# Kernel tuning notes

Hardware: AMD Instinct MI355X
Metric: run time of the kernel (lower is better)

## Reference

```python
import jax, jax.numpy as jnp
import numpy as np

D_MODEL = 1024
D_K = 64
D_V = 64
N_HEADS = 16
LN_EPS = 1e-5


def setup_inputs() -> dict:
    key = jax.random.key(0)
    ks = jax.random.split(key, 9)
    B, S = 2, 2048
    scale = 0.02
    return {
        "input_Q": jax.random.normal(ks[0], (B, S, D_MODEL), dtype=jnp.float32),
        "input_K": jax.random.normal(ks[1], (B, S, D_MODEL), dtype=jnp.float32),
        "input_V": jax.random.normal(ks[2], (B, S, D_MODEL), dtype=jnp.float32),
        "W_Q": jax.random.normal(ks[3], (D_MODEL, N_HEADS * D_K), dtype=jnp.float32) * scale,
        "W_K": jax.random.normal(ks[4], (D_MODEL, N_HEADS * D_K), dtype=jnp.float32) * scale,
        "W_V": jax.random.normal(ks[5], (D_MODEL, N_HEADS * D_V), dtype=jnp.float32) * scale,
        "W_O": jax.random.normal(ks[6], (N_HEADS * D_V, D_MODEL), dtype=jnp.float32) * scale,
        "ln_gamma": jnp.ones((D_MODEL,), dtype=jnp.float32),
        "ln_beta": jnp.zeros((D_MODEL,), dtype=jnp.float32),
    }


def reference(input_Q, input_K, input_V, W_Q, W_K, W_V, W_O, ln_gamma, ln_beta):
    B, Lq, _ = input_Q.shape
    Lk = input_K.shape[1]
    # projections -> [B, H, L, d]
    Q = (input_Q @ W_Q).reshape(B, Lq, N_HEADS, D_K).transpose(0, 2, 1, 3)
    K = (input_K @ W_K).reshape(B, Lk, N_HEADS, D_K).transpose(0, 2, 1, 3)
    V = (input_V @ W_V).reshape(B, Lk, N_HEADS, D_V).transpose(0, 2, 1, 3)
    # scores: [B, H, Lq, Lk]
    scores = jnp.einsum("bhqd,bhkd->bhqk", Q, K) / jnp.sqrt(jnp.float32(D_K))
    # NOTE: source uses nn.Softmax(dim=1) -> softmax over the HEADS axis (faithful quirk)
    attn = jax.nn.softmax(scores, axis=1)
    context = jnp.einsum("bhqk,bhkv->bhqv", attn, V)
    context = context.transpose(0, 2, 1, 3).reshape(B, Lq, N_HEADS * D_V)
    output = context @ W_O
    # residual + LayerNorm over last dim
    x = output + input_Q
    mu = jnp.mean(x, axis=-1, keepdims=True)
    var = jnp.mean(jnp.square(x - mu), axis=-1, keepdims=True)
    return (x - mu) / jnp.sqrt(var + LN_EPS) * ln_gamma + ln_beta
```

## Files before the change

### kernel.cpp

```cpp
#include <hip/hip_runtime.h>
#include <cstdint>
#include <cstddef>

#define DM 1024
#define HEADS 16
#define DHEAD 64
#define SEQ 2048
#define BATCH 2

typedef __bf16 bf16x8 __attribute__((ext_vector_type(8)));
typedef float  f32x4  __attribute__((ext_vector_type(4)));
typedef unsigned short u16;
typedef unsigned int u32;
typedef u16 u16x8 __attribute__((ext_vector_type(8)));
typedef u16 u16x4 __attribute__((ext_vector_type(4)));

__device__ __forceinline__ float bf2f(u16 u){
    union { u32 i; float f; } v; v.i = ((u32)u) << 16; return v.f;
}
__device__ __forceinline__ u16 f2bf(float f){
    union { float f; u32 i; } v; v.f = f;
    u32 r = v.i + 0x7FFF + ((v.i >> 16) & 1);
    return (u16)(r >> 16);
}
__device__ __forceinline__ u16 f2bf_rhu(float f){
    union { float f; u32 i; } v; v.f = f;
    return (u16)((v.i + 0x8000u) >> 16);
}
__device__ __forceinline__ float fexp2(float x){
    float r;
    asm volatile("v_exp_f32 %0, %1\n\ts_nop 1" : "=v"(r) : "v"(x));
    return r;
}
__device__ __forceinline__ void gload16(const u16* g, u16* l){
    __builtin_amdgcn_global_load_lds(
        (const __attribute__((address_space(1))) u32*)g,
        (__attribute__((address_space(3))) u32*)l, 16, 0, 0);
}

__global__ void k_probe(const u16* __restrict__ q, int* __restrict__ hdr){
    if (threadIdx.x == 0 && blockIdx.x == 0){
        int cnt = 0;
        for (int i = 0; i < 256; i += 2){
            int e = (q[i] >> 7) & 0xFF;
            if (e >= 90 && e <= 141) cnt++;
        }
        hdr[0] = (cnt >= 64) ? 1 : 0;
        #pragma unroll
        for (int c = 1; c <= 24; c++) hdr[c] = 0;
    }
}

__global__ __launch_bounds__(256) void k_cvt3(const void* __restrict__ s0,
                                              const void* __restrict__ s1,
                                              const void* __restrict__ s2,
                                              u16* __restrict__ dstbase,
                                              const int* __restrict__ flag, int n){
    int z = blockIdx.y;
    const void* src = (z == 0) ? s0 : ((z == 1) ? s1 : s2);
    u16* dst = dstbase + (size_t)z * n;
    int i = (blockIdx.x * 256 + threadIdx.x) * 8;
    if (i >= n) return;
    if (*flag){
        *(u16x8*)&dst[i] = *(const u16x8*)((const u16*)src + i);
    } else {
        const float* s = (const float*)src + i;
        u16x8 o;
        #pragma unroll
        for (int j = 0; j < 8; j++) o[j] = f2bf(s[j]);
        *(u16x8*)&dst[i] = o;
    }
}

__global__ void k_tcvt4(const void* __restrict__ w0, const void* __restrict__ w1,
                        const void* __restrict__ w2, const void* __restrict__ w3,
                        u16* __restrict__ dstbase,
                        const int* __restrict__ flag, int R, int C){
    __shared__ u16 tile[32][33];
    int z = blockIdx.z;
    const void* src = (z == 0) ? w0 : ((z == 1) ? w1 : ((z == 2) ? w2 : w3));
    u16* dst = dstbase + (size_t)z * R * C;
    bool isbf = (*flag != 0);
    int c0 = blockIdx.x * 32, r0 = blockIdx.y * 32;
    int tx = threadIdx.x, ty = threadIdx.y;
    #pragma unroll
    for (int i = 0; i < 32; i += 8){
        size_t idx = (size_t)(r0 + ty + i) * C + c0 + tx;
        tile[ty + i][tx] = isbf ? ((const u16*)src)[idx] : f2bf(((const float*)src)[idx]);
    }
    __syncthreads();
    #pragma unroll
    for (int i = 0; i < 32; i += 8)
        dst[(size_t)(c0 + ty + i) * R + r0 + tx] = tile[tx][ty + i];
}

__global__ void k_transpose(const u16* __restrict__ src, u16* __restrict__ dst,
                            int R, int C){
    __shared__ u16 tile[32][33];
    size_t boff = (size_t)blockIdx.z * R * C;
    src += boff; dst += boff;
    int c0 = blockIdx.x * 32, r0 = blockIdx.y * 32;
    int tx = threadIdx.x, ty = threadIdx.y;
    #pragma unroll
    for (int i = 0; i < 32; i += 8)
        tile[ty + i][tx] = src[(size_t)(r0 + ty + i) * C + c0 + tx];
    __syncthreads();
    #pragma unroll
    for (int i = 0; i < 32; i += 8)
        dst[(size_t)(c0 + ty + i) * R + r0 + tx] = tile[tx][ty + i];
}

template<int NJ>
__global__ __launch_bounds__(256, 2) void k_gemmT(const u16* __restrict__ A0,
                                                  const u16* __restrict__ Bt0,
                                                  u16* __restrict__ C0,
                                                  size_t strA, size_t strB, size_t strC,
                                                  int M, int N, int K){
    constexpr int BN = NJ * 32;
    __shared__ u16 lsA[128 * 64];
    __shared__ u16 lsB[BN * 64];
    int z = blockIdx.z;
    const u16* A  = A0  + strA * z;
    const u16* Bt = Bt0 + strB * z;
    u16* C = C0 + strC * z;
    int m0 = blockIdx.y * 128, n0 = blockIdx.x * BN;
    int t = threadIdx.x, lane = t & 63, w = t >> 6;
    int l15 = lane & 15, quad = lane >> 4;
    int wm = (w & 1) * 64, wn = (w >> 1) * (NJ * 16);
    f32x4 acc[4][NJ] = {};
    for (int k0 = 0; k0 < K; k0 += 64){
        __syncthreads();
        #pragma unroll
        for (int j = 0; j < 4; j++){
            int ub = j * 256 + w * 64;
            int u  = ub + lane;
            int r  = u >> 3, cg = (u & 7) ^ (r & 7);
            gload16(&A[(size_t)(m0 + r) * K + k0 + cg * 8], &lsA[ub * 8]);
        }
        #pragma unroll
        for (int j = 0; j < NJ; j++){
            int ub = j * 256 + w * 64;
            int u  = ub + lane;
            int r  = u >> 3, cg = (u & 7) ^ (r & 7);
            gload16(&Bt[(size_t)(n0 + r) * K + k0 + cg * 8], &lsB[ub * 8]);
        }
        __syncthreads();
        bf16x8 af[4][2], bfr[NJ][2];
        #pragma unroll
        for (int i = 0; i < 4; i++){
            int row = wm + i * 16 + l15;
            #pragma unroll
            for (int kk = 0; kk < 2; kk++)
                af[i][kk] = *(const bf16x8*)&lsA[row * 64 + (((kk * 4 + quad) ^ (row & 7)) * 8)];
        }
        #pragma unroll
        for (int jj = 0; jj < NJ; jj++){
            int row = wn + jj * 16 + l15;
            #pragma unroll
            for (int kk = 0; kk < 2; kk++)
                bfr[jj][kk] = *(const bf16x8*)&lsB[row * 64 + (((kk * 4 + quad) ^ (row & 7)) * 8)];
        }
        #pragma unroll
        for (int i = 0; i < 4; i++)
            #pragma unroll
            for (int jj = 0; jj < NJ; jj++)
                #pragma unroll
                for (int kk = 0; kk < 2; kk++)
                    acc[i][jj] = __builtin_amdgcn_mfma_f32_16x16x32_bf16(af[i][kk], bfr[jj][kk],
                                                                         acc[i][jj], 0, 0, 0);
    }
    #pragma unroll
    for (int i = 0; i < 4; i++)
        #pragma unroll
        for (int jj = 0; jj < NJ; jj++)
            #pragma unroll
            for (int r = 0; r < 4; r++){
                int m = m0 + wm + i * 16 + quad * 4 + r;
                int n = n0 + wn + jj * 16 + l15;
                C[(size_t)m * N + n] = f2bf(acc[i][jj][r]);
            }
}

__global__ __launch_bounds__(1024, 4) void k_attn5(const u16* __restrict__ Qp,
                                                   const u16* __restrict__ Kp,
                                                   const u16* __restrict__ Vt,
                                                   u16* __restrict__ c0,
                                                   u16* __restrict__ c1,
                                                   u16* __restrict__ c2,
                                                   u16* __restrict__ c3,
                                                   int* __restrict__ cnt,
                                                   int ncomboM1, int iters){
    __shared__ u16 ebuf[2][16][64][36];
    __shared__ int s_combo, s_slot;
    int t = threadIdx.x;
    if (t == 0){
        int xcc;
        asm volatile("s_getreg_b32 %0, hwreg(HW_REG_XCC_ID)" : "=s"(xcc));
        int start = xcc & ncomboM1;
        int combo = -1, slot = -1;
        for (int a = 0; a <= ncomboM1 && combo < 0; a++){
            int c = (start + a) & ncomboM1;
            int s = atomicAdd(&cnt[c], 1);
            if (s < 32){ combo = c; slot = s; }
        }
        s_combo = combo; s_slot = slot;
    }
    __syncthreads();
    int combo = s_combo;
    if (combo < 0) return;
    int b = combo & 1, chunk = combo >> 1;
    int q0 = s_slot * 64;
    int h = t >> 6, lane = t & 63, l15 = lane & 15, quad = lane >> 4;
    u16* outp = (chunk == 0) ? c0 : ((chunk == 1) ? c1 : ((chunk == 2) ? c2 : c3));
    const float cexp = 0.125f * 1.44269504f;
    int kbeg = chunk * (iters << 5);

    bf16x8 qf[4][2];
    #pragma unroll
    for (int sub = 0; sub < 4; sub++)
        #pragma unroll
        for (int ch = 0; ch < 2; ch++)
            qf[sub][ch] = *(const bf16x8*)&Qp[((size_t)(b * SEQ + q0 + sub * 16 + l15)) * DM
                                             + h * DHEAD + ch * 32 + quad * 8];

    f32x4 oacc[4][4] = {};
    int sq = t >> 4, sku = (t & 15) * 2;

    auto score_phase = [&](int it){
        int k0 = kbeg + (it << 5), bf = it & 1;
        #pragma unroll
        for (int kt = 0; kt < 2; kt++){
            const u16* kb = Kp + ((size_t)(b * SEQ + k0 + kt * 16 + l15)) * DM + h * DHEAD + quad * 8;
            bf16x8 kf0 = *(const bf16x8*)(kb);
            bf16x8 kf1 = *(const bf16x8*)(kb + 32);
            #pragma unroll
            for (int sub = 0; sub < 4; sub++){
                f32x4 sc = {};
                sc = __builtin_amdgcn_mfma_f32_16x16x32_bf16(qf[sub][0], kf0, sc, 0, 0, 0);
                sc = __builtin_amdgcn_mfma_f32_16x16x32_bf16(qf[sub][1], kf1, sc, 0, 0, 0);
                #pragma unroll
                for (int r = 0; r < 4; r++)
                    ebuf[bf][h][sub * 16 + quad * 4 + r][kt * 16 + l15] =
                        f2bf_rhu(fexp2(sc[r] * cexp));
            }
        }
    };

    score_phase(0);
    for (int it = 0; it < iters; it++){
        int bf = it & 1;
        __syncthreads();
        {
            u32 ev[16];
            float s0 = 0.f, s1 = 0.f;
            #pragma unroll
            for (int hh = 0; hh < 16; hh++){
                u32 u = *(const u32*)&ebuf[bf][hh][sq][sku];
                ev[hh] = u;
                union { u32 i; float f; } lo, hi;
                lo.i = u << 16; hi.i = u & 0xFFFF0000u;
                s0 += lo.f; s1 += hi.f;
            }
            float r0 = __builtin_amdgcn_rcpf(s0);
            float r1 = __builtin_amdgcn_rcpf(s1);
            #pragma unroll
            for (int hh = 0; hh < 16; hh++){
                union { u32 i; float f; } lo, hi, p0, p1;
                lo.i = ev[hh] << 16; hi.i = ev[hh] & 0xFFFF0000u;
                p0.f = lo.f * r0; p1.f = hi.f * r1;
                *(u32*)&ebuf[bf][hh][sq][sku] =
                    __builtin_amdgcn_perm(p1.i + 0x8000u, p0.i + 0x8000u, 0x07060302u);
            }
        }
        __syncthreads();
        int k0 = kbeg + (it << 5);
        bf16x8 pa[4];
        #pragma unroll
        for (int sub = 0; sub < 4; sub++){
            const u16* pp = &ebuf[bf][h][sub * 16 + l15][quad * 8];
            union { bf16x8 v; u16x4 q[2]; } pu;
            pu.q[0] = *(const u16x4*)pp;
            pu.q[1] = *(const u16x4*)(pp + 4);
            pa[sub] = pu.v;
        }
        #pragma unroll
        for (int vt = 0; vt < 4; vt++){
            bf16x8 vf = *(const bf16x8*)&Vt[((size_t)b * DM + h * DHEAD + vt * 16 + l15) * SEQ
                                            + k0 + quad * 8];
            #pragma unroll
            for (int sub = 0; sub < 4; sub++)
                oacc[sub][vt] = __builtin_amdgcn_mfma_f32_16x16x32_bf16(pa[sub], vf, oacc[sub][vt], 0, 0, 0);
        }
        if (it + 1 < iters) score_phase(it + 1);
    }
    #pragma unroll
    for (int sub = 0; sub < 4; sub++)
        #pragma unroll
        for (int vt = 0; vt < 4; vt++)
            #pragma unroll
            for (int r = 0; r < 4; r++){
                int q = q0 + sub * 16 + quad * 4 + r;
                int n = h * DHEAD + vt * 16 + l15;
                outp[((size_t)b * SEQ + q) * DM + n] = f2bf(oacc[sub][vt][r]);
            }
}

__global__ __launch_bounds__(256) void k_reduce(const u16* __restrict__ a,
                                                const u16* __restrict__ b,
                                                const u16* __restrict__ c,
                                                const u16* __restrict__ d,
                                                u16* __restrict__ dst, int n, int nch){
    int i = (blockIdx.x * 256 + threadIdx.x) * 8;
    if (i >= n) return;
    u16x8 x = *(const u16x8*)&a[i];
    u16x8 y = *(const u16x8*)&b[i];
    u16x8 o;
    if (nch == 4){
        u16x8 zc = *(const u16x8*)&c[i];
        u16x8 zd = *(const u16x8*)&d[i];
        #pragma unroll
        for (int j = 0; j < 8; j++)
            o[j] = f2bf((bf2f(x[j]) + bf2f(y[j])) + (bf2f(zc[j]) + bf2f(zd[j])));
    } else {
        #pragma unroll
        for (int j = 0; j < 8; j++) o[j] = f2bf(bf2f(x[j]) + bf2f(y[j]));
    }
    *(u16x8*)&dst[i] = o;
}

__global__ __launch_bounds__(256) void k_ln(const u16* __restrict__ O,
                                            const void* __restrict__ Qin,
                                            const void* __restrict__ gamma,
                                            const void* __restrict__ beta,
                                            void* __restrict__ out,
                                            const int* __restrict__ flag){
    __shared__ float red[4][2];
    bool isbf = (*flag != 0);
    int row = blockIdx.x;
    int t = threadIdx.x;
    const u16* op = O + (size_t)row * DM;
    float xv[4];
    float s1 = 0.f, s2 = 0.f;
    #pragma unroll
    for (int i = 0; i < 4; i++){
        int idx = i * 256 + t;
        float q = isbf ? bf2f(((const u16*)Qin)[(size_t)row * DM + idx])
                       : ((const float*)Qin)[(size_t)row * DM + idx];
        float x = bf2f(op[idx]) + q;
        xv[i] = x; s1 += x; s2 += x * x;
    }
    #pragma unroll
    for (int off = 32; off; off >>= 1){
        s1 += __shfl_down(s1, off);
        s2 += __shfl_down(s2, off);
    }
    int w = t >> 6, lane = t & 63;
    if (lane == 0){ red[w][0] = s1; red[w][1] = s2; }
    __syncthreads();
    float S1 = red[0][0] + red[1][0] + red[2][0] + red[3][0];
    float S2 = red[0][1] + red[1][1] + red[2][1] + red[3][1];
    float mu  = S1 * (1.0f / DM);
    float var = S2 * (1.0f / DM) - mu * mu;
    float rstd = rsqrtf(var + 1e-5f);
    #pragma unroll
    for (int i = 0; i < 4; i++){
        int idx = i * 256 + t;
        float g = isbf ? bf2f(((const u16*)gamma)[idx]) : ((const float*)gamma)[idx];
        float bb= isbf ? bf2f(((const u16*)beta )[idx]) : ((const float*)beta )[idx];
        float y = (xv[i] - mu) * rstd * g + bb;
        if (isbf) ((u16*)out)[(size_t)row * DM + idx] = f2bf(y);
        else      ((float*)out)[(size_t)row * DM + idx] = y;
    }
}

extern "C" void kernel_launch(void* const* d_in, const int* in_sizes, int n_in,
                              void* d_out, int out_size, void* d_ws, size_t ws_size,
                              hipStream_t stream){
    (void)in_sizes; (void)n_in; (void)out_size;
    const void* inQ = d_in[0];
    const void* inK = d_in[1];
    const void* inV = d_in[2];
    const void* wQ  = d_in[3];
    const void* wK  = d_in[4];
    const void* wV  = d_in[5];
    const void* wO  = d_in[6];
    const void* gma = d_in[7];
    const void* bta = d_in[8];

    int* hdr  = (int*)d_ws;
    int* flag = hdr;
    int* cnt  = hdr + 1;
    u16* base = (u16*)d_ws + 64;

    const size_t MB1 = 1024u * 1024u;
    const size_t M4  = 4u * MB1;
    u16* Qi  = base + 0;
    u16* Ki  = base + 1 * M4;
    u16* Vi  = base + 2 * M4;
    u16* WtQ = base + 3 * M4;
    u16* WtO = WtQ + 3 * MB1;
    u16* Qp  = base + 4 * M4;
    u16* Kp  = base + 5 * M4;
    u16* Vp  = base + 6 * M4;
    u16* ext = base + 7 * M4;
    u16* Vt    = Ki;
    u16* ctxp0 = Qi;
    u16* ctxp1 = Vp;
    u16* ctxp2 = Vi;

    size_t need4 = 128 + 8 * M4 * sizeof(u16);
    int nch = (ws_size >= need4) ? 4 : 2;
    u16* ctxp3 = (nch == 4) ? ext : ctxp2;
    int ncomboM1 = 2 * nch - 1;
    int iters   = (nch == 4) ? 16 : 32;
    int ablocks = 32 * 2 * nch;

    k_probe<<<1, 64, 0, stream>>>((const u16*)inQ, hdr);

    const int nIn = BATCH * SEQ * DM;
    k_cvt3<<<dim3(nIn / 2048, 3), 256, 0, stream>>>(inQ, inK, inV, base, flag, nIn);

    k_tcvt4<<<dim3(32, 32, 4), dim3(32, 8), 0, stream>>>(wQ, wK, wV, wO, WtQ, flag, 1024, 1024);

    k_gemmT<4><<<dim3(8, 32, 3), 256, 0, stream>>>(Qi, WtQ, Qp, M4, MB1, M4, 4096, 1024, 1024);

    k_transpose<<<dim3(32, 64, 2), dim3(32, 8), 0, stream>>>(Vp, Vt, 2048, 1024);

    k_attn5<<<ablocks, 1024, 0, stream>>>(Qp, Kp, Vt, ctxp0, ctxp1, ctxp2, ctxp3,
                                          cnt, ncomboM1, iters);

    k_reduce<<<nIn / 2048, 256, 0, stream>>>(ctxp0, ctxp1, ctxp2, ctxp3, ctxp0, nIn, nch);

    k_gemmT<2><<<dim3(16, 32, 1), 256, 0, stream>>>(ctxp0, WtO, Qp, 0, 0, 0, 4096, 1024, 1024);

    k_ln<<<4096, 256, 0, stream>>>(Qp, inQ, gma, bta, d_out, flag);
}
```

Before: 319.8 us.

## Fuse dtype probe into convert kernel and compute V projection pre-transposed

Drops the single-thread probe kernel: every thread of the input-convert kernel now re-derives the bf16/fp32 flag from a smaller sample, and block 0 writes the header. Drops the separate V transpose by computing V^T directly as W_V^T times input_V^T with a second GEMM launch per batch. This removes two launches and a full read and write of the V projection, in exchange for a GEMM with a less favourable shape and a weaker dtype heuristic over fewer samples.

```diff
diff --git a/kernel.cpp b/kernel.cpp
--- a/kernel.cpp
+++ b/kernel.cpp
@@ -37,31 +37,33 @@
         (const __attribute__((address_space(1))) u32*)g,
         (__attribute__((address_space(3))) u32*)l, 16, 0, 0);
 }
-
-__global__ void k_probe(const u16* __restrict__ q, int* __restrict__ hdr){
-    if (threadIdx.x == 0 && blockIdx.x == 0){
-        int cnt = 0;
-        for (int i = 0; i < 256; i += 2){
-            int e = (q[i] >> 7) & 0xFF;
-            if (e >= 90 && e <= 141) cnt++;
-        }
-        hdr[0] = (cnt >= 64) ? 1 : 0;
-        #pragma unroll
-        for (int c = 1; c <= 24; c++) hdr[c] = 0;
-    }
+__device__ __forceinline__ int probe_flag(const u16* q){
+    int cnt = 0;
+    #pragma unroll
+    for (int i = 0; i < 32; i += 2){
+        int e = (q[i] >> 7) & 0xFF;
+        if (e >= 90 && e <= 141) cnt++;
+    }
+    return (cnt >= 12) ? 1 : 0;
 }
 
 __global__ __launch_bounds__(256) void k_cvt3(const void* __restrict__ s0,
                                               const void* __restrict__ s1,
                                               const void* __restrict__ s2,
                                               u16* __restrict__ dstbase,
-                                              const int* __restrict__ flag, int n){
+                                              int* __restrict__ hdr, int n){
+    int isbf = probe_flag((const u16*)s0);
+    if (blockIdx.x == 0 && blockIdx.y == 0 && threadIdx.x == 0){
+        hdr[0] = isbf;
+        #pragma unroll
+        for (int c = 1; c <= 24; c++) hdr[c] = 0;
+    }
     int z = blockIdx.y;
     const void* src = (z == 0) ? s0 : ((z == 1) ? s1 : s2);
     u16* dst = dstbase + (size_t)z * n;
     int i = (blockIdx.x * 256 + threadIdx.x) * 8;
     if (i >= n) return;
-    if (*flag){
+    if (isbf){
         *(u16x8*)&dst[i] = *(const u16x8*)((const u16*)src + i);
     } else {
         const float* s = (const float*)src + i;
@@ -88,22 +90,6 @@
         size_t idx = (size_t)(r0 + ty + i) * C + c0 + tx;
         tile[ty + i][tx] = isbf ? ((const u16*)src)[idx] : f2bf(((const float*)src)[idx]);
     }
-    __syncthreads();
-    #pragma unroll
-    for (int i = 0; i < 32; i += 8)
-        dst[(size_t)(c0 + ty + i) * R + r0 + tx] = tile[tx][ty + i];
-}
-
-__global__ void k_transpose(const u16* __restrict__ src, u16* __restrict__ dst,
-                            int R, int C){
-    __shared__ u16 tile[32][33];
-    size_t boff = (size_t)blockIdx.z * R * C;
-    src += boff; dst += boff;
-    int c0 = blockIdx.x * 32, r0 = blockIdx.y * 32;
-    int tx = threadIdx.x, ty = threadIdx.y;
-    #pragma unroll
-    for (int i = 0; i < 32; i += 8)
-        tile[ty + i][tx] = src[(size_t)(r0 + ty + i) * C + c0 + tx];
     __syncthreads();
     #pragma unroll
     for (int i = 0; i < 32; i += 8)
@@ -394,10 +380,12 @@
 
     const size_t MB1 = 1024u * 1024u;
     const size_t M4  = 4u * MB1;
+    const size_t M2  = 2u * MB1;
     u16* Qi  = base + 0;
     u16* Ki  = base + 1 * M4;
     u16* Vi  = base + 2 * M4;
     u16* WtQ = base + 3 * M4;
+    u16* WtV = WtQ + 2 * MB1;
     u16* WtO = WtQ + 3 * MB1;
     u16* Qp  = base + 4 * M4;
     u16* Kp  = base + 5 * M4;
@@ -415,16 +403,14 @@
     int iters   = (nch == 4) ? 16 : 32;
     int ablocks = 32 * 2 * nch;
 
-    k_probe<<<1, 64, 0, stream>>>((const u16*)inQ, hdr);
-
     const int nIn = BATCH * SEQ * DM;
-    k_cvt3<<<dim3(nIn / 2048, 3), 256, 0, stream>>>(inQ, inK, inV, base, flag, nIn);
+    k_cvt3<<<dim3(nIn / 2048, 3), 256, 0, stream>>>(inQ, inK, inV, base, hdr, nIn);
 
     k_tcvt4<<<dim3(32, 32, 4), dim3(32, 8), 0, stream>>>(wQ, wK, wV, wO, WtQ, flag, 1024, 1024);
 
-    k_gemmT<4><<<dim3(8, 32, 3), 256, 0, stream>>>(Qi, WtQ, Qp, M4, MB1, M4, 4096, 1024, 1024);
-
-    k_transpose<<<dim3(32, 64, 2), dim3(32, 8), 0, stream>>>(Vp, Vt, 2048, 1024);
+    k_gemmT<4><<<dim3(8, 32, 2), 256, 0, stream>>>(Qi, WtQ, Qp, M4, MB1, M4, 4096, 1024, 1024);
+
+    k_gemmT<2><<<dim3(32, 8, 2), 256, 0, stream>>>(WtV, Vi, Vt, 0, M2, M2, 1024, 2048, 1024);
 
     k_attn5<<<ablocks, 1024, 0, stream>>>(Qp, Kp, Vt, ctxp0, ctxp1, ctxp2, ctxp3,
                                           cnt, ncomboM1, iters);
```

Measured after the change: 316.6 us. No clear change (-1.0%).
